# Kernel tuning notes

Hardware: AMD Instinct MI355X
Metric: run time of the kernel (lower is better)

Reference implementation:

```python
import jax, jax.numpy as jnp
import numpy as np

N, E, F_IN, HID, HEADS, C, NCLS, NG, NCONV = 50000, 800000, 128, 128, 8, 16, 10, 64, 3
EPS = 1e-5
NEG_SLOPE = 0.2


def bn_eval(x, p):
    # p: [4, dim] = (gamma, beta, running_mean, running_var); eval-mode BatchNorm1d
    g, b, m, v = p[0], p[1], p[2], p[3]
    return g * (x - m) * jax.lax.rsqrt(v + EPS) + b


def gat_conv(x, src, dst, W, a_src, a_dst, bias):
    # PyG GATConv, concat=True, add_self_loops=True, eval (no dropout)
    h = (x @ W).reshape(N, HEADS, C)                    # [N,H,C]
    alpha_s = jnp.sum(h * a_src[None], axis=-1)         # [N,H]
    alpha_d = jnp.sum(h * a_dst[None], axis=-1)         # [N,H]
    loop = jnp.arange(N)
    s = jnp.concatenate([src, loop])                    # [E+N]
    d = jnp.concatenate([dst, loop])
    logits = jax.nn.leaky_relu(alpha_s[s] + alpha_d[d], NEG_SLOPE)   # [E+N,H]
    mx = jax.lax.stop_gradient(jax.ops.segment_max(logits, d, num_segments=N))
    ex = jnp.exp(logits - mx[d])
    denom = jax.ops.segment_sum(ex, d, num_segments=N)
    alpha = ex / (denom[d] + 1e-16)                     # segment softmax over dst
    msg = h[s] * alpha[:, :, None]                      # [E+N,H,C]
    out = jax.ops.segment_sum(msg, d, num_segments=N)   # [N,H,C]
    return out.reshape(N, HEADS * C) + bias


def setup_inputs() -> dict:
    key = jax.random.key(0)
    ks = jax.random.split(key, 16)

    def bn_p(dim):
        return jnp.stack([jnp.ones(dim), jnp.full((dim,), 1e-4), jnp.zeros(dim), jnp.ones(dim)])

    sc = 0.05
    inp = {
        "x": jax.random.normal(ks[0], (N, F_IN), jnp.float32),
        "edge_index": jax.random.randint(ks[1], (2, E), 0, N),
        "batch": jnp.sort(jax.random.randint(ks[2], (N,), 0, NG)),
        "bn_feat_params": bn_p(F_IN),
        "w_feat": jax.random.normal(ks[3], (F_IN, HID), jnp.float32) * sc,
        "b_feat": jnp.zeros((HID,), jnp.float32),
        "bns_conv_params": jnp.stack([bn_p(HID)] * NCONV),
        "gat_w": jax.random.normal(ks[4], (NCONV, HID, HID), jnp.float32) * sc,
        "gat_att_src": jax.random.normal(ks[5], (NCONV, HEADS, C), jnp.float32) * sc,
        "gat_att_dst": jax.random.normal(ks[6], (NCONV, HEADS, C), jnp.float32) * sc,
        "gat_b": jnp.zeros((NCONV, HID), jnp.float32),
        "bns_fc_params": jnp.stack([bn_p(HID)] * 1),
        "fc_w": jax.random.normal(ks[7], (1, HID, HID), jnp.float32) * sc,
        "fc_b": jnp.zeros((1, HID), jnp.float32),
        "bn_hidden_params": bn_p(HID),
        "w_class": jax.random.normal(ks[8], (HID, NCLS), jnp.float32) * sc,
        "b_class": jnp.zeros((NCLS,), jnp.float32),
    }
    return inp


def reference(x, edge_index, batch, bn_feat_params, w_feat, b_feat, bns_conv_params,
              gat_w, gat_att_src, gat_att_dst, gat_b, bns_fc_params, fc_w, fc_b,
              bn_hidden_params, w_class, b_class):
    src, dst = edge_index[0], edge_index[1]
    h = bn_eval(x, bn_feat_params)
    h = jax.nn.relu(h @ w_feat + b_feat)             # GCNConv(gfn=True) == linear
    for i in range(NCONV):
        h = bn_eval(h, bns_conv_params[i])
        h = jax.nn.relu(gat_conv(h, src, dst, gat_w[i], gat_att_src[i], gat_att_dst[i], gat_b[i]))
    g = jax.ops.segment_sum(h, batch, num_segments=NG)   # global_add_pool -> [NG,HID]
    for i in range(fc_w.shape[0]):
        g = jax.nn.relu(bn_eval(g, bns_fc_params[i]) @ fc_w[i] + fc_b[i])
    g = bn_eval(g, bn_hidden_params)
    logits = g @ w_class + b_class
    return jax.nn.log_softmax(logits, axis=-1)
```

## Files before the change

### kernel.cpp

```cpp
#include <hip/hip_runtime.h>

#define NN 50000
#define E_EDGES 800000
#define F_INN 128
#define HIDD 128
#define HEADS 8
#define CDIM 16
#define NCLS 10
#define NGG 64
#define NCONV 3
#define EPSS 1e-5f
#define NEG_SLOPE 0.2f

#define WROWS 144
#define WSTRIDE (WROWS * 128)
#define BSTRIDE 144

#define BSH 7
#define BSZ 128
#define NB ((NN + BSZ - 1) / BSZ)
#define BIN_BLOCKS 256
#define BIN_CHUNK (E_EDGES / BIN_BLOCKS)
#define TABW 392
#define CAPB 4608
#define SORT_BUF 4608
#define PW_KCH 32
#define GTILES ((NN + 127) / 128)
#define TPITCH 132

typedef __attribute__((ext_vector_type(8))) short short8;
typedef __attribute__((ext_vector_type(4))) float f32x4;
typedef __attribute__((ext_vector_type(2))) float f32x2;

__device__ __forceinline__ float lrelu(float x) { return x > 0.f ? x : NEG_SLOPE * x; }

__device__ __forceinline__ float bf2f(ushort u) {
    union { unsigned int i; float f; } v;
    v.i = ((unsigned int)u) << 16;
    return v.f;
}
__device__ __forceinline__ ushort f2bf(float f) {
    union { float f; unsigned int i; } v;
    v.f = f;
    unsigned int r = (v.i + 0x7fffu + ((v.i >> 16) & 1u)) >> 16;
    return (ushort)r;
}
__device__ __forceinline__ unsigned char f2fp8(float f) {
    int r = __builtin_amdgcn_cvt_pk_fp8_f32(f, f, 0, false);
    return (unsigned char)(r & 0xff);
}

__device__ __forceinline__ void gemm_core_l0(int tile, int t,
    const float* __restrict__ Ain, const ushort* __restrict__ Wt,
    const float* __restrict__ bias, ushort* __restrict__ Out, int n)
{
    int wave = t >> 6, lane = t & 63;
    int m16 = lane & 15, quad = lane >> 4;
    int rbase = tile * 128 + wave * 32;

    short8 afrag[2][4];
    #pragma unroll
    for (int tt = 0; tt < 2; ++tt) {
        int arow_i = rbase + tt * 16 + m16;
        size_t arow = (size_t)(arow_i < n ? arow_i : 0) * HIDD + quad * 8;
        const float* ap = Ain + arow;
        #pragma unroll
        for (int kk = 0; kk < 4; ++kk) {
            float4 lo = *(const float4*)(ap + kk * 32);
            float4 hi = *(const float4*)(ap + kk * 32 + 4);
            short8 f;
            f[0] = (short)f2bf(lo.x); f[1] = (short)f2bf(lo.y);
            f[2] = (short)f2bf(lo.z); f[3] = (short)f2bf(lo.w);
            f[4] = (short)f2bf(hi.x); f[5] = (short)f2bf(hi.y);
            f[6] = (short)f2bf(hi.z); f[7] = (short)f2bf(hi.w);
            afrag[tt][kk] = f;
        }
    }

    f32x4 acc[2][8];
    #pragma unroll
    for (int tt = 0; tt < 2; ++tt)
        #pragma unroll
        for (int nt = 0; nt < 8; ++nt) acc[tt][nt] = (f32x4){0.f, 0.f, 0.f, 0.f};

    #pragma unroll
    for (int nt = 0; nt < 8; ++nt) {
        const ushort* brow = Wt + (size_t)(nt * 16 + m16) * HIDD + quad * 8;
        #pragma unroll
        for (int kk = 0; kk < 4; ++kk) {
            short8 bfrag = *(const short8*)(brow + kk * 32);
            acc[0][nt] = __builtin_amdgcn_mfma_f32_16x16x32_bf16(afrag[0][kk], bfrag, acc[0][nt], 0, 0, 0);
            acc[1][nt] = __builtin_amdgcn_mfma_f32_16x16x32_bf16(afrag[1][kk], bfrag, acc[1][nt], 0, 0, 0);
        }
    }

    #pragma unroll
    for (int tt = 0; tt < 2; ++tt) {
        int tb = rbase + tt * 16;
        #pragma unroll
        for (int nt = 0; nt < 8; ++nt) {
            int col = nt * 16 + m16;
            float bv = bias[col];
            #pragma unroll
            for (int r = 0; r < 4; ++r) {
                int orow = tb + quad * 4 + r;
                if (orow < n) {
                    float v = fmaxf(acc[tt][nt][r] + bv, 0.f);
                    Out[(size_t)orow * HIDD + col] = f2bf(v);
                }
            }
        }
    }
}

__global__ __launch_bounds__(256) void prep_bin(
    const float* __restrict__ bn_feat, const float* __restrict__ w_feat,
    const float* __restrict__ b_feat, const float* __restrict__ bns_conv,
    const float* __restrict__ gat_w, const float* __restrict__ att_src,
    const float* __restrict__ att_dst, const int* __restrict__ src,
    const int* __restrict__ dst, ushort* __restrict__ Wt,
    float* __restrict__ bp, unsigned int* __restrict__ tmp, int* __restrict__ tab)
{
    __shared__ __align__(16) char smem[18560];
    int blk = blockIdx.x;
    int t = threadIdx.x;

    if (blk < 16) {
        float* Wl = (float*)smem;
        float* aak = Wl + PW_KCH * 129;
        int layer = blk >> 2;
        int k0 = (blk & 3) * PW_KCH;
        const float* bn; const float* W;
        if (layer == 0) { bn = bn_feat; W = w_feat; }
        else { bn = bns_conv + (layer - 1) * 4 * HIDD; W = gat_w + (size_t)(layer - 1) * HIDD * HIDD; }
        if (t < PW_KCH) {
            int k = k0 + t;
            aak[t] = bn[k] * rsqrtf(bn[3 * HIDD + k] + EPSS);
        }
        for (int i = t; i < PW_KCH * 128; i += 256) {
            int kk = i >> 7, n = i & 127;
            Wl[kk * 129 + n] = W[(size_t)(k0 + kk) * 128 + n];
        }
        __syncthreads();
        ushort* wrow = Wt + (size_t)layer * WSTRIDE;
        for (int i = t; i < 128 * PW_KCH; i += 256) {
            int n = i >> 5, kk = i & 31;
            wrow[n * 128 + k0 + kk] = f2bf(aak[kk] * Wl[kk * 129 + n]);
        }
    } else if (blk < 20) {
        float* ccs = (float*)smem;
        int layer = blk - 16;
        const float* bn; const float* W;
        if (layer == 0) { bn = bn_feat; W = w_feat; }
        else { bn = bns_conv + (layer - 1) * 4 * HIDD; W = gat_w + (size_t)(layer - 1) * HIDD * HIDD; }
        if (t < 128) {
            float a = bn[t] * rsqrtf(bn[3 * HIDD + t] + EPSS);
            ccs[t] = bn[HIDD + t] - bn[2 * HIDD + t] * a;
        }
        __syncthreads();
        if (t < 128) {
            float bacc = (layer == 0) ? b_feat[t] : 0.f;
            for (int k = 0; k < 128; ++k) bacc += ccs[k] * W[(size_t)k * 128 + t];
            bp[layer * BSTRIDE + t] = bacc;
        }
    } else if (blk < 23) {
        float* Wl   = (float*)smem;
        float* redS = (float*)(smem + 16512);
        float* redD = redS + 256;
        int li = blk - 20;
        int L = li + 1;
        const float* bn = bns_conv + li * 4 * HIDD;
        const float* W  = gat_w + (size_t)li * HIDD * HIDD;
        const float* as = att_src + li * HEADS * CDIM;
        const float* ad = att_dst + li * HEADS * CDIM;
        ushort* Wo = Wt + (size_t)L * WSTRIDE;
        int kl = t >> 3, h = t & 7;
        float acc_s = 0.f, acc_d = 0.f;
        for (int c0 = 0; c0 < 4; ++c0) {
            int k0 = c0 * 32;
            __syncthreads();
            for (int i = t; i < 32 * 128; i += 256) {
                int kk = i >> 7, n = i & 127;
                Wl[kk * 129 + n] = W[(size_t)(k0 + kk) * 128 + n];
            }
            __syncthreads();
            int k = k0 + kl;
            float a  = bn[k] * rsqrtf(bn[3 * HIDD + k] + EPSS);
            float cc = bn[HIDD + k] - bn[2 * HIDD + k] * a;
            float ps = 0.f, pd = 0.f;
            #pragma unroll
            for (int c = 0; c < 16; ++c) {
                float wv = Wl[kl * 129 + h * 16 + c];
                ps += wv * as[h * 16 + c];
                pd += wv * ad[h * 16 + c];
            }
            Wo[(128 + h) * 128 + k] = f2bf(a * ps);
            Wo[(136 + h) * 128 + k] = f2bf(a * pd);
            acc_s += cc * ps;
            acc_d += cc * pd;
        }
        redS[t] = acc_s; redD[t] = acc_d;
        __syncthreads();
        if (t < 8) {
            float s = 0.f, d = 0.f;
            for (int q = 0; q < 32; ++q) { s += redS[q * 8 + t]; d += redD[q * 8 + t]; }
            bp[L * BSTRIDE + 128 + t] = s;
            bp[L * BSTRIDE + 136 + t] = d;
        }
    } else {
        unsigned int* stage = (unsigned int*)smem;
        int* hist = (int*)(smem + 12512);
        int* A    = hist + TABW;
        int k = blk - 23;
        int cbeg = k * BIN_CHUNK;
        int cend = cbeg + BIN_CHUNK;

        for (int i = t; i < TABW; i += 256) hist[i] = 0;
        __syncthreads();
        for (int e = cbeg + t; e < cend; e += 256)
            atomicAdd(&hist[dst[e] >> BSH], 1);
        __syncthreads();
        int i1 = t + 256;
        int c0 = hist[t];
        int c1 = (i1 < TABW) ? hist[i1] : 0;
        A[t] = c0; A[i1] = c1;
        __syncthreads();
        for (int d = 1; d < 512; d <<= 1) {
            int a0 = (t >= d) ? A[t - d] : 0;
            int a1 = A[i1 - d];
            __syncthreads();
            A[t] += a0; A[i1] += a1;
            __syncthreads();
        }
        int e0 = A[t] - c0;
        int e1 = A[i1] - c1;
        tab[(size_t)t * BIN_BLOCKS + k] = e0;
        if (i1 < TABW) tab[(size_t)i1 * BIN_BLOCKS + k] = e1;
        hist[t] = e0;
        if (i1 < TABW) hist[i1] = e1;
        __syncthreads();
        for (int e = cbeg + t; e < cend; e += 256) {
            int d = dst[e];
            int b = d >> BSH;
            unsigned int pk = ((unsigned int)(d & (BSZ - 1)) << 16) | (unsigned int)src[e];
            int p = atomicAdd(&hist[b], 1);
            stage[p] = pk;
        }
        __syncthreads();
        for (int i = t; i < BIN_CHUNK; i += 256)
            tmp[(size_t)k * BIN_CHUNK + i] = stage[i];
    }
}

__global__ __launch_bounds__(256) void sort_gemm0(
    const int* __restrict__ tab, const unsigned int* __restrict__ tmp,
    ushort* __restrict__ csr, unsigned int* __restrict__ rowptr,
    const float* __restrict__ x, const ushort* __restrict__ Wt,
    const float* __restrict__ bp, ushort* __restrict__ h_a)
{
    int t = threadIdx.x;
    if (blockIdx.x < NB) {
        __shared__ unsigned int buf[SORT_BUF];
        __shared__ int sc[256];
        __shared__ int o0s[256];
        __shared__ int hist[BSZ], pex[BSZ], cur[BSZ];
        int b = blockIdx.x;
        int base_out = b * CAPB;

        int o0 = tab[(size_t)b * BIN_BLOCKS + t];
        int o1 = tab[(size_t)(b + 1) * BIN_BLOCKS + t];
        int c = o1 - o0;
        o0s[t] = o0;
        sc[t] = c;
        __syncthreads();
        for (int d = 1; d < 256; d <<= 1) {
            int a = (t >= d) ? sc[t - d] : 0;
            __syncthreads();
            sc[t] += a;
            __syncthreads();
        }
        int m = sc[255];
        int mybase = sc[t] - c;
        if (m > CAPB - BSZ * 7) m = CAPB - BSZ * 7;
        for (int j = 0; j < c; ++j) {
            int p = mybase + j;
            if (p < m) buf[p] = tmp[(size_t)t * BIN_CHUNK + o0s[t] + j];
        }
        if (t < BSZ) hist[t] = 0;
        __syncthreads();
        for (int i = t; i < m; i += 256) atomicAdd(&hist[buf[i] >> 16], 1);
        __syncthreads();
        int pd = 0;
        if (t < BSZ) { pd = (hist[t] + 7) & ~7; pex[t] = pd; }
        __syncthreads();
        for (int d = 1; d < BSZ; d <<= 1) {
            int a = (t < BSZ && t >= d) ? pex[t - d] : 0;
            __syncthreads();
            if (t < BSZ) pex[t] += a;
            __syncthreads();
        }
        if (t < BSZ) {
            int ex = pex[t] - pd;
            pex[t] = ex;
            cur[t] = ex;
            int node = b * BSZ + t;
            if (node < NN)
                rowptr[node] = (unsigned int)(base_out + ex) | ((unsigned int)hist[t] << 21);
        }
        __syncthreads();
        for (int i = t; i < m; i += 256) {
            unsigned int pk = buf[i];
            int dl = pk >> 16;
            int p = atomicAdd(&cur[dl], 1);
            csr[base_out + p] = (ushort)(pk & 0xffffu);
        }
        __syncthreads();
        if (t < BSZ) {
            int ex = pex[t], hn = hist[t], pdn = (hn + 7) & ~7;
            for (int i = hn; i < pdn; ++i) csr[base_out + ex + i] = 0;
        }
    } else {
        gemm_core_l0(blockIdx.x - NB, t, x, Wt, bp, h_a, NN);
    }
}

__global__ __launch_bounds__(256) void gemm_conv(const ushort* __restrict__ Ain,
    const ushort* __restrict__ Wt, const float* __restrict__ bias,
    unsigned char* __restrict__ h8, float* __restrict__ alph_s,
    float* __restrict__ alph_d)
{
    __shared__ unsigned char tile[128 * TPITCH];
    int t = threadIdx.x;
    int wave = t >> 6, lane = t & 63;
    int m16 = lane & 15, quad = lane >> 4;
    int tile0 = blockIdx.x * 128;
    int rbase = tile0 + wave * 32;
    const int n = NN;

    short8 afrag[2][4];
    #pragma unroll
    for (int tt = 0; tt < 2; ++tt) {
        int arow_i = rbase + tt * 16 + m16;
        size_t arow = (size_t)(arow_i < n ? arow_i : 0) * HIDD + quad * 8;
        const ushort* ap = Ain + arow;
        #pragma unroll
        for (int kk = 0; kk < 4; ++kk)
            afrag[tt][kk] = *(const short8*)(ap + kk * 32);
    }

    f32x4 acc[2][9];
    #pragma unroll
    for (int tt = 0; tt < 2; ++tt)
        #pragma unroll
        for (int nt = 0; nt < 9; ++nt) acc[tt][nt] = (f32x4){0.f, 0.f, 0.f, 0.f};

    #pragma unroll
    for (int nt = 0; nt < 9; ++nt) {
        const ushort* brow = Wt + (size_t)(nt * 16 + m16) * HIDD + quad * 8;
        #pragma unroll
        for (int kk = 0; kk < 4; ++kk) {
            short8 bfrag = *(const short8*)(brow + kk * 32);
            acc[0][nt] = __builtin_amdgcn_mfma_f32_16x16x32_bf16(afrag[0][kk], bfrag, acc[0][nt], 0, 0, 0);
            acc[1][nt] = __builtin_amdgcn_mfma_f32_16x16x32_bf16(afrag[1][kk], bfrag, acc[1][nt], 0, 0, 0);
        }
    }

    #pragma unroll
    for (int tt = 0; tt < 2; ++tt) {
        int lrow = wave * 32 + tt * 16;
        #pragma unroll
        for (int nt = 0; nt < 8; ++nt) {
            int col = nt * 16 + m16;
            float bv = bias[col];
            #pragma unroll
            for (int r = 0; r < 4; ++r) {
                float v = acc[tt][nt][r] + bv;
                tile[(lrow + quad * 4 + r) * TPITCH + col] = f2fp8(v);
            }
        }
        {
            float bv = bias[128 + m16];
            int tb = rbase + tt * 16;
            #pragma unroll
            for (int r = 0; r < 4; ++r) {
                int orow = tb + quad * 4 + r;
                if (orow < n) {
                    float v = acc[tt][8][r] + bv;
                    if (m16 < 8) alph_s[orow * HEADS + m16] = v;
                    else         alph_d[orow * HEADS + (m16 - 8)] = v;
                }
            }
        }
    }
    __syncthreads();
    {
        int row = t >> 1, half = t & 1;
        int orow = tile0 + row;
        if (orow < n) {
            const unsigned char* srcp = &tile[row * TPITCH + half * 64];
            uint4* dstp = (uint4*)(h8 + (size_t)orow * HIDD + half * 64);
            #pragma unroll
            for (int j = 0; j < 4; ++j)
                dstp[j] = *(const uint4*)(srcp + j * 16);
        }
    }
}

__global__ __launch_bounds__(256) void gat_aggregate(
    const unsigned char* __restrict__ h8,
    const float* __restrict__ as, const float* __restrict__ ad,
    const unsigned int* __restrict__ rowptr, const ushort* __restrict__ csr,
    const float* __restrict__ bias, ushort* __restrict__ out)
{
    int wid = (blockIdx.x * 256 + threadIdx.x) >> 6;
    int v = __builtin_amdgcn_readfirstlane(wid);
    if (v >= NN) return;
    int lane = threadIdx.x & 63;
    int hd = lane >> 3;
    int slot = lane & 7;
    int half = lane >> 5;
    int li = lane & 31;
    int chh = li >> 2;

    unsigned int rp = rowptr[v];
    int beg = rp & 0x1FFFFF;
    int cnt = rp >> 21;
    float adv = ad[v * HEADS + hd];

    const unsigned int* h32 = (const unsigned int*)h8;

    float wself = __expf(lrelu(as[v * HEADS + hd] + adv));
    float wself_ch = __shfl(wself, chh * 8, 64);
    unsigned int sx = h32[(size_t)v * 32 + li];
    f32x2 sl = __builtin_amdgcn_cvt_pk_f32_fp8((int)sx, false);
    f32x2 sh = __builtin_amdgcn_cvt_pk_f32_fp8((int)sx, true);
    float selfm = half ? 0.f : wself_ch;
    float acc0 = selfm * sl[0], acc1 = selfm * sl[1];
    float acc2 = selfm * sh[0], acc3 = selfm * sh[1];
    float wsum_own = 0.f;

    int ngro = (cnt + 7) >> 3;
    if (ngro > 0) {
        const uint4* epk = (const uint4*)(csr + beg);
        float l_own0, l_own1;
        int u0[4], u1[4];
        unsigned int x0[4], x1[4];
        {
            uint4 pk = epk[0];
            u0[0] = half ? (int)(pk.x >> 16) : (int)(pk.x & 0xffff);
            u0[1] = half ? (int)(pk.y >> 16) : (int)(pk.y & 0xffff);
            u0[2] = half ? (int)(pk.z >> 16) : (int)(pk.z & 0xffff);
            u0[3] = half ? (int)(pk.w >> 16) : (int)(pk.w & 0xffff);
            unsigned int d = slot < 4 ? (slot < 2 ? pk.x : pk.y)
                                      : (slot < 6 ? pk.z : pk.w);
            int u_own = (slot & 1) ? (int)(d >> 16) : (int)(d & 0xffff);
            l_own0 = as[u_own * HEADS + hd];
            #pragma unroll
            for (int j = 0; j < 4; ++j) x0[j] = h32[(size_t)u0[j] * 32 + li];
        }
        for (int g = 0; g < ngro; ++g) {
            bool more = (g + 1 < ngro);
            if (more) {
                uint4 pk = epk[g + 1];
                u1[0] = half ? (int)(pk.x >> 16) : (int)(pk.x & 0xffff);
                u1[1] = half ? (int)(pk.y >> 16) : (int)(pk.y & 0xffff);
                u1[2] = half ? (int)(pk.z >> 16) : (int)(pk.z & 0xffff);
                u1[3] = half ? (int)(pk.w >> 16) : (int)(pk.w & 0xffff);
                unsigned int d = slot < 4 ? (slot < 2 ? pk.x : pk.y)
                                          : (slot < 6 ? pk.z : pk.w);
                int u_own = (slot & 1) ? (int)(d >> 16) : (int)(d & 0xffff);
                l_own1 = as[u_own * HEADS + hd];
                #pragma unroll
                for (int j = 0; j < 4; ++j) x1[j] = h32[(size_t)u1[j] * 32 + li];
            }
            float w_own = __expf(lrelu(l_own0 + adv));
            if (g * 8 + slot >= cnt) w_own = 0.f;
            wsum_own += w_own;
            #pragma unroll
            for (int j = 0; j < 4; ++j) {
                float wj = __shfl(w_own, chh * 8 + 2 * j + half, 64);
                f32x2 lo = __builtin_amdgcn_cvt_pk_f32_fp8((int)x0[j], false);
                f32x2 hi = __builtin_amdgcn_cvt_pk_f32_fp8((int)x0[j], true);
                acc0 += wj * lo[0];
                acc1 += wj * lo[1];
                acc2 += wj * hi[0];
                acc3 += wj * hi[1];
            }
            if (more) {
                l_own0 = l_own1;
                #pragma unroll
                for (int j = 0; j < 4; ++j) { u0[j] = u1[j]; x0[j] = x1[j]; }
            }
        }
    }

    #pragma unroll
    for (int off = 1; off < 8; off <<= 1) wsum_own += __shfl_xor(wsum_own, off);
    float denom = wself + wsum_own;
    float inv_hd = 1.f / (denom + 1e-16f);
    float inv = __shfl(inv_hd, chh * 8, 64);

    acc0 += __shfl_xor(acc0, 32);
    acc1 += __shfl_xor(acc1, 32);
    acc2 += __shfl_xor(acc2, 32);
    acc3 += __shfl_xor(acc3, 32);

    float sa = half ? acc2 : acc0;
    float sb = half ? acc3 : acc1;
    int c0 = 4 * li + 2 * half;
    float o0 = fmaxf(sa * inv + bias[c0], 0.f);
    float o1 = fmaxf(sb * inv + bias[c0 + 1], 0.f);
    ((unsigned int*)out)[(size_t)v * 64 + 2 * li + half] =
        (unsigned int)f2bf(o0) | ((unsigned int)f2bf(o1) << 16);
}

__global__ __launch_bounds__(256) void pool_head(const ushort* __restrict__ h,
    const int* __restrict__ batch,
    const float* __restrict__ bns_fc, const float* __restrict__ fc_w,
    const float* __restrict__ fc_b, const float* __restrict__ bn_hid,
    const float* __restrict__ w_class, const float* __restrict__ b_class,
    float* __restrict__ out)
{
    __shared__ float sred[2048];
    __shared__ float v1[HIDD];
    __shared__ float v2[HIDD];
    __shared__ float lg[NCLS];
    __shared__ float lse;
    __shared__ int bounds[2];
    int gb = blockIdx.x, t = threadIdx.x;

    if (t < 2) {
        int key = gb + t;
        int lo = 0, hi = NN;
        while (lo < hi) {
            int mid = (lo + hi) >> 1;
            if (batch[mid] < key) lo = mid + 1; else hi = mid;
        }
        bounds[t] = lo;
    }
    __syncthreads();
    int beg = bounds[0], end = bounds[1];

    int rg = t >> 4, cg = t & 15;
    float a[8] = {0.f, 0.f, 0.f, 0.f, 0.f, 0.f, 0.f, 0.f};
    for (int r = beg + rg; r < end; r += 16) {
        short8 vv = *(const short8*)(h + (size_t)r * HIDD + cg * 8);
        #pragma unroll
        for (int k = 0; k < 8; ++k) a[k] += bf2f((ushort)vv[k]);
    }
    #pragma unroll
    for (int k = 0; k < 8; ++k) sred[rg * 128 + cg * 8 + k] = a[k];
    __syncthreads();

    if (t < HIDD) {
        float gv = 0.f;
        #pragma unroll
        for (int q = 0; q < 16; ++q) gv += sred[q * 128 + t];
        float gamma = bns_fc[t], beta = bns_fc[HIDD + t];
        float mu = bns_fc[2 * HIDD + t], var = bns_fc[3 * HIDD + t];
        v1[t] = (gv - mu) * gamma * rsqrtf(var + EPSS) + beta;
    }
    __syncthreads();

    if (t < HIDD) {
        float acc = fc_b[t];
        for (int k = 0; k < HIDD; ++k) acc += v1[k] * fc_w[k * HIDD + t];
        acc = fmaxf(acc, 0.f);
        float gamma = bn_hid[t], beta = bn_hid[HIDD + t];
        float mu = bn_hid[2 * HIDD + t], var = bn_hid[3 * HIDD + t];
        v2[t] = (acc - mu) * gamma * rsqrtf(var + EPSS) + beta;
    }
    __syncthreads();

    if (t < NCLS) {
        float acc2 = b_class[t];
        for (int k = 0; k < HIDD; ++k) acc2 += v2[k] * w_class[k * NCLS + t];
        lg[t] = acc2;
    }
    __syncthreads();
    if (t == 0) {
        float mx = lg[0];
        for (int i = 1; i < NCLS; ++i) mx = fmaxf(mx, lg[i]);
        float ss = 0.f;
        for (int i = 0; i < NCLS; ++i) ss += __expf(lg[i] - mx);
        lse = mx + __logf(ss);
    }
    __syncthreads();
    if (t < NCLS) out[gb * NCLS + t] = lg[t] - lse;
}

extern "C" void kernel_launch(void* const* d_in, const int* in_sizes, int n_in,
                              void* d_out, int out_size, void* d_ws, size_t ws_size,
                              hipStream_t stream)
{
    const float* x        = (const float*)d_in[0];
    const int*   edge     = (const int*)d_in[1];
    const int*   batch    = (const int*)d_in[2];
    const float* bn_feat  = (const float*)d_in[3];
    const float* w_feat   = (const float*)d_in[4];
    const float* b_feat   = (const float*)d_in[5];
    const float* bns_conv = (const float*)d_in[6];
    const float* gat_w    = (const float*)d_in[7];
    const float* att_src  = (const float*)d_in[8];
    const float* att_dst  = (const float*)d_in[9];
    const float* gat_b    = (const float*)d_in[10];
    const float* bns_fc   = (const float*)d_in[11];
    const float* fc_w     = (const float*)d_in[12];
    const float* fc_b     = (const float*)d_in[13];
    const float* bn_hid   = (const float*)d_in[14];
    const float* w_class  = (const float*)d_in[15];
    const float* b_class  = (const float*)d_in[16];
    float* out = (float*)d_out;
    (void)in_sizes; (void)n_in; (void)out_size; (void)ws_size;

    char* ws = (char*)d_ws;
    size_t off = 0;
    auto alloc = [&](size_t bytes) {
        void* p = ws + off;
        off = (off + bytes + 255) & ~(size_t)255;
        return p;
    };
    ushort* Wt        = (ushort*)alloc((size_t)4 * WSTRIDE * sizeof(ushort));
    float*  bp        = (float*)alloc(4 * BSTRIDE * sizeof(float));
    ushort* h_a       = (ushort*)alloc((size_t)NN * HIDD * sizeof(ushort));
    unsigned char* h8 = (unsigned char*)alloc((size_t)NN * HIDD);
    float*  alph_s    = (float*)alloc((size_t)NN * HEADS * sizeof(float));
    float*  alph_d    = (float*)alloc((size_t)NN * HEADS * sizeof(float));
    int*    tab       = (int*)alloc((size_t)BIN_BLOCKS * TABW * sizeof(int));
    unsigned int* tmp = (unsigned int*)alloc((size_t)E_EDGES * sizeof(unsigned int));
    unsigned int* rowptr = (unsigned int*)alloc((size_t)NN * sizeof(unsigned int));
    ushort* csr       = (ushort*)alloc((size_t)NB * CAPB * sizeof(ushort) + 64);

    const int* src = edge;
    const int* dst = edge + E_EDGES;

    prep_bin<<<279, 256, 0, stream>>>(bn_feat, w_feat, b_feat, bns_conv, gat_w,
                                      att_src, att_dst, src, dst, Wt, bp, tmp, tab);
    sort_gemm0<<<NB + GTILES, 256, 0, stream>>>(tab, tmp, csr, rowptr,
                                                x, Wt, bp, h_a);

    for (int i = 0; i < NCONV; ++i) {
        gemm_conv<<<GTILES, 256, 0, stream>>>(h_a,
            Wt + (size_t)(i + 1) * WSTRIDE, bp + (i + 1) * BSTRIDE, h8,
            alph_s, alph_d);
        gat_aggregate<<<(NN + 3) / 4, 256, 0, stream>>>(h8, alph_s, alph_d,
                                                        rowptr, csr, gat_b + i * HIDD, h_a);
    }

    pool_head<<<NGG, 256, 0, stream>>>(h_a, batch, bns_fc, fc_w, fc_b, bn_hid,
                                       w_class, b_class, out);
}
```

Before: 293.5 us.

## Replace two-level binning scan with global atomic bucket append

Result: slower. 558.9 us (+90.4%).

```diff
diff --git a/kernel.cpp b/kernel.cpp
--- a/kernel.cpp
+++ b/kernel.cpp
@@ -21,9 +21,8 @@
 #define NB ((NN + BSZ - 1) / BSZ)
 #define BIN_BLOCKS 256
 #define BIN_CHUNK (E_EDGES / BIN_BLOCKS)
-#define TABW 392
 #define CAPB 4608
-#define SORT_BUF 4608
+#define MCLAMP (CAPB - BSZ * 7)
 #define PW_KCH 32
 #define GTILES ((NN + 127) / 128)
 #define TPITCH 132
@@ -119,7 +118,8 @@
     const float* __restrict__ gat_w, const float* __restrict__ att_src,
     const float* __restrict__ att_dst, const int* __restrict__ src,
     const int* __restrict__ dst, ushort* __restrict__ Wt,
-    float* __restrict__ bp, unsigned int* __restrict__ tmp, int* __restrict__ tab)
+    float* __restrict__ bp, unsigned int* __restrict__ raw,
+    unsigned int* __restrict__ cnt)
 {
     __shared__ __align__(16) char smem[18560];
     int blk = blockIdx.x;
@@ -208,84 +208,36 @@
             bp[L * BSTRIDE + 136 + t] = d;
         }
     } else {
-        unsigned int* stage = (unsigned int*)smem;
-        int* hist = (int*)(smem + 12512);
-        int* A    = hist + TABW;
         int k = blk - 23;
         int cbeg = k * BIN_CHUNK;
         int cend = cbeg + BIN_CHUNK;
-
-        for (int i = t; i < TABW; i += 256) hist[i] = 0;
-        __syncthreads();
-        for (int e = cbeg + t; e < cend; e += 256)
-            atomicAdd(&hist[dst[e] >> BSH], 1);
-        __syncthreads();
-        int i1 = t + 256;
-        int c0 = hist[t];
-        int c1 = (i1 < TABW) ? hist[i1] : 0;
-        A[t] = c0; A[i1] = c1;
-        __syncthreads();
-        for (int d = 1; d < 512; d <<= 1) {
-            int a0 = (t >= d) ? A[t - d] : 0;
-            int a1 = A[i1 - d];
-            __syncthreads();
-            A[t] += a0; A[i1] += a1;
-            __syncthreads();
-        }
-        int e0 = A[t] - c0;
-        int e1 = A[i1] - c1;
-        tab[(size_t)t * BIN_BLOCKS + k] = e0;
-        if (i1 < TABW) tab[(size_t)i1 * BIN_BLOCKS + k] = e1;
-        hist[t] = e0;
-        if (i1 < TABW) hist[i1] = e1;
-        __syncthreads();
         for (int e = cbeg + t; e < cend; e += 256) {
             int d = dst[e];
             int b = d >> BSH;
             unsigned int pk = ((unsigned int)(d & (BSZ - 1)) << 16) | (unsigned int)src[e];
-            int p = atomicAdd(&hist[b], 1);
-            stage[p] = pk;
-        }
-        __syncthreads();
-        for (int i = t; i < BIN_CHUNK; i += 256)
-            tmp[(size_t)k * BIN_CHUNK + i] = stage[i];
+            unsigned int p = atomicAdd(&cnt[b], 1u);
+            if (p < CAPB) raw[(size_t)b * CAPB + p] = pk;
+        }
     }
 }
 
 __global__ __launch_bounds__(256) void sort_gemm0(
-    const int* __restrict__ tab, const unsigned int* __restrict__ tmp,
+    const unsigned int* __restrict__ cnt, const unsigned int* __restrict__ raw,
     ushort* __restrict__ csr, unsigned int* __restrict__ rowptr,
     const float* __restrict__ x, const ushort* __restrict__ Wt,
     const float* __restrict__ bp, ushort* __restrict__ h_a)
 {
     int t = threadIdx.x;
     if (blockIdx.x < NB) {
-        __shared__ unsigned int buf[SORT_BUF];
-        __shared__ int sc[256];
-        __shared__ int o0s[256];
+        __shared__ unsigned int buf[CAPB];
         __shared__ int hist[BSZ], pex[BSZ], cur[BSZ];
         int b = blockIdx.x;
         int base_out = b * CAPB;
 
-        int o0 = tab[(size_t)b * BIN_BLOCKS + t];
-        int o1 = tab[(size_t)(b + 1) * BIN_BLOCKS + t];
-        int c = o1 - o0;
-        o0s[t] = o0;
-        sc[t] = c;
-        __syncthreads();
-        for (int d = 1; d < 256; d <<= 1) {
-            int a = (t >= d) ? sc[t - d] : 0;
-            __syncthreads();
-            sc[t] += a;
-            __syncthreads();
-        }
-        int m = sc[255];
-        int mybase = sc[t] - c;
-        if (m > CAPB - BSZ * 7) m = CAPB - BSZ * 7;
-        for (int j = 0; j < c; ++j) {
-            int p = mybase + j;
-            if (p < m) buf[p] = tmp[(size_t)t * BIN_CHUNK + o0s[t] + j];
-        }
+        int m = (int)cnt[b];
+        if (m > MCLAMP) m = MCLAMP;
+
+        for (int i = t; i < m; i += 256) buf[i] = raw[(size_t)b * CAPB + i];
         if (t < BSZ) hist[t] = 0;
         __syncthreads();
         for (int i = t; i < m; i += 256) atomicAdd(&hist[buf[i] >> 16], 1);
@@ -626,17 +578,19 @@
     unsigned char* h8 = (unsigned char*)alloc((size_t)NN * HIDD);
     float*  alph_s    = (float*)alloc((size_t)NN * HEADS * sizeof(float));
     float*  alph_d    = (float*)alloc((size_t)NN * HEADS * sizeof(float));
-    int*    tab       = (int*)alloc((size_t)BIN_BLOCKS * TABW * sizeof(int));
-    unsigned int* tmp = (unsigned int*)alloc((size_t)E_EDGES * sizeof(unsigned int));
+    unsigned int* cnt = (unsigned int*)alloc((size_t)NB * sizeof(unsigned int));
+    unsigned int* raw = (unsigned int*)alloc((size_t)NB * CAPB * sizeof(unsigned int));
     unsigned int* rowptr = (unsigned int*)alloc((size_t)NN * sizeof(unsigned int));
     ushort* csr       = (ushort*)alloc((size_t)NB * CAPB * sizeof(ushort) + 64);
 
     const int* src = edge;
     const int* dst = edge + E_EDGES;
 
+    hipMemsetAsync(cnt, 0, (size_t)NB * sizeof(unsigned int), stream);
+
     prep_bin<<<279, 256, 0, stream>>>(bn_feat, w_feat, b_feat, bns_conv, gat_w,
-                                      att_src, att_dst, src, dst, Wt, bp, tmp, tab);
-    sort_gemm0<<<NB + GTILES, 256, 0, stream>>>(tab, tmp, csr, rowptr,
+                                      att_src, att_dst, src, dst, Wt, bp, raw, cnt);
+    sort_gemm0<<<NB + GTILES, 256, 0, stream>>>(cnt, raw, csr, rowptr,
                                                 x, Wt, bp, h_a);
 
     for (int i = 0; i < NCONV; ++i) {
```

## Fuse global add pool into last GAT aggregation via float atomics

Applied to the files above, without the earlier changes.

New measurement: 390.5 us. 1.33x slower.

```diff
diff --git a/kernel.cpp b/kernel.cpp
--- a/kernel.cpp
+++ b/kernel.cpp
@@ -410,7 +410,8 @@
     const unsigned char* __restrict__ h8,
     const float* __restrict__ as, const float* __restrict__ ad,
     const unsigned int* __restrict__ rowptr, const ushort* __restrict__ csr,
-    const float* __restrict__ bias, ushort* __restrict__ out)
+    const float* __restrict__ bias, ushort* __restrict__ out,
+    float* __restrict__ gpool, const int* __restrict__ batch, int last)
 {
     int wid = (blockIdx.x * 256 + threadIdx.x) >> 6;
     int v = __builtin_amdgcn_readfirstlane(wid);
@@ -510,52 +511,30 @@
     int c0 = 4 * li + 2 * half;
     float o0 = fmaxf(sa * inv + bias[c0], 0.f);
     float o1 = fmaxf(sb * inv + bias[c0 + 1], 0.f);
-    ((unsigned int*)out)[(size_t)v * 64 + 2 * li + half] =
-        (unsigned int)f2bf(o0) | ((unsigned int)f2bf(o1) << 16);
-}
-
-__global__ __launch_bounds__(256) void pool_head(const ushort* __restrict__ h,
-    const int* __restrict__ batch,
+    if (last) {
+        int bg = batch[v];
+        atomicAdd(&gpool[bg * HIDD + c0], o0);
+        atomicAdd(&gpool[bg * HIDD + c0 + 1], o1);
+    } else {
+        ((unsigned int*)out)[(size_t)v * 64 + 2 * li + half] =
+            (unsigned int)f2bf(o0) | ((unsigned int)f2bf(o1) << 16);
+    }
+}
+
+__global__ __launch_bounds__(256) void pool_head(const float* __restrict__ gpool,
     const float* __restrict__ bns_fc, const float* __restrict__ fc_w,
     const float* __restrict__ fc_b, const float* __restrict__ bn_hid,
     const float* __restrict__ w_class, const float* __restrict__ b_class,
     float* __restrict__ out)
 {
-    __shared__ float sred[2048];
     __shared__ float v1[HIDD];
     __shared__ float v2[HIDD];
     __shared__ float lg[NCLS];
     __shared__ float lse;
-    __shared__ int bounds[2];
     int gb = blockIdx.x, t = threadIdx.x;
 
-    if (t < 2) {
-        int key = gb + t;
-        int lo = 0, hi = NN;
-        while (lo < hi) {
-            int mid = (lo + hi) >> 1;
-            if (batch[mid] < key) lo = mid + 1; else hi = mid;
-        }
-        bounds[t] = lo;
-    }
-    __syncthreads();
-    int beg = bounds[0], end = bounds[1];
-
-    int rg = t >> 4, cg = t & 15;
-    float a[8] = {0.f, 0.f, 0.f, 0.f, 0.f, 0.f, 0.f, 0.f};
-    for (int r = beg + rg; r < end; r += 16) {
-        short8 vv = *(const short8*)(h + (size_t)r * HIDD + cg * 8);
-        #pragma unroll
-        for (int k = 0; k < 8; ++k) a[k] += bf2f((ushort)vv[k]);
-    }
-    #pragma unroll
-    for (int k = 0; k < 8; ++k) sred[rg * 128 + cg * 8 + k] = a[k];
-    __syncthreads();
-
     if (t < HIDD) {
-        float gv = 0.f;
-        #pragma unroll
-        for (int q = 0; q < 16; ++q) gv += sred[q * 128 + t];
+        float gv = gpool[gb * HIDD + t];
         float gamma = bns_fc[t], beta = bns_fc[HIDD + t];
         float mu = bns_fc[2 * HIDD + t], var = bns_fc[3 * HIDD + t];
         v1[t] = (gv - mu) * gamma * rsqrtf(var + EPSS) + beta;
@@ -630,9 +609,12 @@
     unsigned int* tmp = (unsigned int*)alloc((size_t)E_EDGES * sizeof(unsigned int));
     unsigned int* rowptr = (unsigned int*)alloc((size_t)NN * sizeof(unsigned int));
     ushort* csr       = (ushort*)alloc((size_t)NB * CAPB * sizeof(ushort) + 64);
+    float*  gpool     = (float*)alloc((size_t)NGG * HIDD * sizeof(float));
 
     const int* src = edge;
     const int* dst = edge + E_EDGES;
+
+    hipMemsetAsync(gpool, 0, (size_t)NGG * HIDD * sizeof(float), stream);
 
     prep_bin<<<279, 256, 0, stream>>>(bn_feat, w_feat, b_feat, bns_conv, gat_w,
                                       att_src, att_dst, src, dst, Wt, bp, tmp, tab);
@@ -644,9 +626,10 @@
             Wt + (size_t)(i + 1) * WSTRIDE, bp + (i + 1) * BSTRIDE, h8,
             alph_s, alph_d);
         gat_aggregate<<<(NN + 3) / 4, 256, 0, stream>>>(h8, alph_s, alph_d,
-                                                        rowptr, csr, gat_b + i * HIDD, h_a);
-    }
-
-    pool_head<<<NGG, 256, 0, stream>>>(h_a, batch, bns_fc, fc_w, fc_b, bn_hid,
+                                                        rowptr, csr, gat_b + i * HIDD, h_a,
+                                                        gpool, batch, (i == NCONV - 1) ? 1 : 0);
+    }
+
+    pool_head<<<NGG, 256, 0, stream>>>(gpool, bns_fc, fc_w, fc_b, bn_hid,
                                        w_class, b_class, out);
 }
```

## Remap GAT aggregation lanes so each lane owns one edge-head with 16-byte gathers

Applied to the files above, without the earlier changes.

Result: slower. 314.2 us (+7.0%).

```diff
diff --git a/kernel.cpp b/kernel.cpp
--- a/kernel.cpp
+++ b/kernel.cpp
@@ -416,102 +416,97 @@
     int v = __builtin_amdgcn_readfirstlane(wid);
     if (v >= NN) return;
     int lane = threadIdx.x & 63;
-    int hd = lane >> 3;
-    int slot = lane & 7;
-    int half = lane >> 5;
-    int li = lane & 31;
-    int chh = li >> 2;
+    int h = lane & 7;
+    int slot = lane >> 3;
 
     unsigned int rp = rowptr[v];
     int beg = rp & 0x1FFFFF;
     int cnt = rp >> 21;
-    float adv = ad[v * HEADS + hd];
-
-    const unsigned int* h32 = (const unsigned int*)h8;
-
-    float wself = __expf(lrelu(as[v * HEADS + hd] + adv));
-    float wself_ch = __shfl(wself, chh * 8, 64);
-    unsigned int sx = h32[(size_t)v * 32 + li];
-    f32x2 sl = __builtin_amdgcn_cvt_pk_f32_fp8((int)sx, false);
-    f32x2 sh = __builtin_amdgcn_cvt_pk_f32_fp8((int)sx, true);
-    float selfm = half ? 0.f : wself_ch;
-    float acc0 = selfm * sl[0], acc1 = selfm * sl[1];
-    float acc2 = selfm * sh[0], acc3 = selfm * sh[1];
-    float wsum_own = 0.f;
+    float adv = ad[v * HEADS + h];
+    float wself = __expf(lrelu(as[v * HEADS + h] + adv));
+
+    const uint4* h16 = (const uint4*)h8;
+
+    float acc[16];
+    {
+        uint4 sx = h16[(size_t)v * 8 + h];
+        float selfm = (slot == 0) ? wself : 0.f;
+        const unsigned int* sw = (const unsigned int*)&sx;
+        #pragma unroll
+        for (int q = 0; q < 4; ++q) {
+            f32x2 lo = __builtin_amdgcn_cvt_pk_f32_fp8((int)sw[q], false);
+            f32x2 hi = __builtin_amdgcn_cvt_pk_f32_fp8((int)sw[q], true);
+            acc[4 * q + 0] = selfm * lo[0];
+            acc[4 * q + 1] = selfm * lo[1];
+            acc[4 * q + 2] = selfm * hi[0];
+            acc[4 * q + 3] = selfm * hi[1];
+        }
+    }
+    float wsum = 0.f;
 
     int ngro = (cnt + 7) >> 3;
     if (ngro > 0) {
         const uint4* epk = (const uint4*)(csr + beg);
-        float l_own0, l_own1;
-        int u0[4], u1[4];
-        unsigned int x0[4], x1[4];
+        float l0, l1;
+        uint4 x0, x1;
         {
             uint4 pk = epk[0];
-            u0[0] = half ? (int)(pk.x >> 16) : (int)(pk.x & 0xffff);
-            u0[1] = half ? (int)(pk.y >> 16) : (int)(pk.y & 0xffff);
-            u0[2] = half ? (int)(pk.z >> 16) : (int)(pk.z & 0xffff);
-            u0[3] = half ? (int)(pk.w >> 16) : (int)(pk.w & 0xffff);
             unsigned int d = slot < 4 ? (slot < 2 ? pk.x : pk.y)
                                       : (slot < 6 ? pk.z : pk.w);
-            int u_own = (slot & 1) ? (int)(d >> 16) : (int)(d & 0xffff);
-            l_own0 = as[u_own * HEADS + hd];
-            #pragma unroll
-            for (int j = 0; j < 4; ++j) x0[j] = h32[(size_t)u0[j] * 32 + li];
+            int u = (slot & 1) ? (int)(d >> 16) : (int)(d & 0xffff);
+            l0 = as[u * HEADS + h];
+            x0 = h16[(size_t)u * 8 + h];
         }
         for (int g = 0; g < ngro; ++g) {
             bool more = (g + 1 < ngro);
             if (more) {
                 uint4 pk = epk[g + 1];
-                u1[0] = half ? (int)(pk.x >> 16) : (int)(pk.x & 0xffff);
-                u1[1] = half ? (int)(pk.y >> 16) : (int)(pk.y & 0xffff);
-                u1[2] = half ? (int)(pk.z >> 16) : (int)(pk.z & 0xffff);
-                u1[3] = half ? (int)(pk.w >> 16) : (int)(pk.w & 0xffff);
                 unsigned int d = slot < 4 ? (slot < 2 ? pk.x : pk.y)
                                           : (slot < 6 ? pk.z : pk.w);
-                int u_own = (slot & 1) ? (int)(d >> 16) : (int)(d & 0xffff);
-                l_own1 = as[u_own * HEADS + hd];
-                #pragma unroll
-                for (int j = 0; j < 4; ++j) x1[j] = h32[(size_t)u1[j] * 32 + li];
+                int u = (slot & 1) ? (int)(d >> 16) : (int)(d & 0xffff);
+                l1 = as[u * HEADS + h];
+                x1 = h16[(size_t)u * 8 + h];
             }
-            float w_own = __expf(lrelu(l_own0 + adv));
-            if (g * 8 + slot >= cnt) w_own = 0.f;
-            wsum_own += w_own;
+            float w = __expf(lrelu(l0 + adv));
+            if (g * 8 + slot >= cnt) w = 0.f;
+            wsum += w;
+            const unsigned int* xw = (const unsigned int*)&x0;
             #pragma unroll
-            for (int j = 0; j < 4; ++j) {
-                float wj = __shfl(w_own, chh * 8 + 2 * j + half, 64);
-                f32x2 lo = __builtin_amdgcn_cvt_pk_f32_fp8((int)x0[j], false);
-                f32x2 hi = __builtin_amdgcn_cvt_pk_f32_fp8((int)x0[j], true);
-                acc0 += wj * lo[0];
-                acc1 += wj * lo[1];
-                acc2 += wj * hi[0];
-                acc3 += wj * hi[1];
+            for (int q = 0; q < 4; ++q) {
+                f32x2 lo = __builtin_amdgcn_cvt_pk_f32_fp8((int)xw[q], false);
+                f32x2 hi = __builtin_amdgcn_cvt_pk_f32_fp8((int)xw[q], true);
+                acc[4 * q + 0] += w * lo[0];
+                acc[4 * q + 1] += w * lo[1];
+                acc[4 * q + 2] += w * hi[0];
+                acc[4 * q + 3] += w * hi[1];
             }
-            if (more) {
-                l_own0 = l_own1;
-                #pragma unroll
-                for (int j = 0; j < 4; ++j) { u0[j] = u1[j]; x0[j] = x1[j]; }
-            }
-        }
-    }
-
-    #pragma unroll
-    for (int off = 1; off < 8; off <<= 1) wsum_own += __shfl_xor(wsum_own, off);
-    float denom = wself + wsum_own;
-    float inv_hd = 1.f / (denom + 1e-16f);
-    float inv = __shfl(inv_hd, chh * 8, 64);
-
-    acc0 += __shfl_xor(acc0, 32);
-    acc1 += __shfl_xor(acc1, 32);
-    acc2 += __shfl_xor(acc2, 32);
-    acc3 += __shfl_xor(acc3, 32);
-
-    float sa = half ? acc2 : acc0;
-    float sb = half ? acc3 : acc1;
-    int c0 = 4 * li + 2 * half;
-    float o0 = fmaxf(sa * inv + bias[c0], 0.f);
-    float o1 = fmaxf(sb * inv + bias[c0 + 1], 0.f);
-    ((unsigned int*)out)[(size_t)v * 64 + 2 * li + half] =
-        (unsigned int)f2bf(o0) | ((unsigned int)f2bf(o1) << 16);
+            if (more) { l0 = l1; x0 = x1; }
+        }
+    }
+
+    #pragma unroll
+    for (int off = 8; off < 64; off <<= 1) {
+        wsum += __shfl_xor(wsum, off);
+        #pragma unroll
+        for (int i = 0; i < 16; ++i) acc[i] += __shfl_xor(acc[i], off);
+    }
+    float inv = 1.f / (wself + wsum + 1e-16f);
+
+    if (slot == 0) {
+        int c0 = h * 16;
+        unsigned int wr[8];
+        #pragma unroll
+        for (int i = 0; i < 8; ++i) {
+            float o0 = fmaxf(acc[2 * i]     * inv + bias[c0 + 2 * i],     0.f);
+            float o1 = fmaxf(acc[2 * i + 1] * inv + bias[c0 + 2 * i + 1], 0.f);
+            wr[i] = (unsigned int)f2bf(o0) | ((unsigned int)f2bf(o1) << 16);
+        }
+        uint4* orow = (uint4*)out + (size_t)v * 16 + h * 2;
+        uint4 a; a.x = wr[0]; a.y = wr[1]; a.z = wr[2]; a.w = wr[3];
+        uint4 b; b.x = wr[4]; b.y = wr[5]; b.z = wr[6]; b.w = wr[7];
+        orow[0] = a;
+        orow[1] = b;
+    }
 }
 
 __global__ __launch_bounds__(256) void pool_head(const ushort* __restrict__ h,
```
